# Kernel tuning notes

Measured on AMD Instinct MI355X. Metric: run time of the kernel, lower is better.

## Reference

```python
import jax, jax.numpy as jnp
import numpy as np

N0, N1, N2 = 512, 2048, 8192   # targets, hop1, hop2 node counts
K = 33                          # nneighbor + self loop
IN, HID, OUT, NH = 256, 128, 128, 8
NEG = -9.0e15
ALPHA = 0.2                     # LeakyReLU negative slope


def setup_inputs() -> dict:
    key = jax.random.key(0)
    ks = jax.random.split(key, 8)
    feats = jax.random.normal(ks[0], (N2, IN), jnp.float32)
    # xavier-ish scaled params (gain 1.414)
    W1 = jax.random.normal(ks[1], (NH, IN, HID), jnp.float32) * 0.072
    a1 = jax.random.normal(ks[2], (NH, 2 * HID), jnp.float32) * 0.105
    W2 = jax.random.normal(ks[3], (HID * NH, OUT), jnp.float32) * 0.042
    a2 = jax.random.normal(ks[4], (2 * OUT,), jnp.float32) * 0.105
    # layer1 edges: each of N1 targets gets K distinct neighbors in [0, N2)
    tgt1 = jnp.repeat(jnp.arange(N1, dtype=jnp.int32), K)
    dst1 = ((jnp.arange(N1)[:, None] * 97 + jnp.arange(K)[None, :] * 131) % N2).astype(jnp.int32).reshape(-1)
    src1 = jax.random.randint(ks[5], (N1 * K,), 0, N2, jnp.int32)
    # layer2 edges: each of N0 targets gets K distinct neighbors in [0, N1)
    tgt2 = jnp.repeat(jnp.arange(N0, dtype=jnp.int32), K)
    dst2 = ((jnp.arange(N0)[:, None] * 53 + jnp.arange(K)[None, :] * 61) % N1).astype(jnp.int32).reshape(-1)
    src2 = jax.random.randint(ks[6], (N0 * K,), 0, N1, jnp.int32)
    return dict(feats=feats, W1=W1, a1=a1, W2=W2, a2=a2,
                src1=src1, dst1=dst1, tgt1=tgt1, src2=src2, dst2=dst2, tgt2=tgt2)


def gat_layer(x, W, a, src, dst, tgt, t_len):
    # x: [n, in], W: [in, d], a: [2d]
    h = x @ W                                   # [n, d]
    d = h.shape[1]
    # concat([h[src], h[dst]]) @ a  ==  h[src]@a[:d] + h[dst]@a[d:]
    e = h[src] @ a[:d] + h[dst] @ a[d:]         # [E]
    e = jnp.where(e > 0, e, ALPHA * e)          # LeakyReLU
    att = jnp.full((t_len, h.shape[0]), NEG, h.dtype).at[tgt, dst].set(e)
    att = jax.nn.softmax(att, axis=1)           # dense row softmax (masked entries ~0)
    return jax.nn.elu(att @ h)                  # [t_len, d]


def reference(feats, W1, a1, W2, a2, src1, dst1, tgt1, src2, dst2, tgt2):
    # layer 1: nhead independent GAT heads over hop2 features
    heads = jax.vmap(lambda W, a: gat_layer(feats, W, a, src1, dst1, tgt1, N1))(W1, a1)  # [NH, N1, HID]
    x = jnp.transpose(heads, (1, 0, 2)).reshape(N1, NH * HID)  # torch.cat(dim=1)
    # layer 2: single GAT layer producing [N0, OUT]
    return gat_layer(x, W2, a2, src2, dst2, tgt2, N0)
```

## Files before the change

### kernel.cpp

```cpp
#include <hip/hip_runtime.h>
#include <math.h>

#define ALPHA 0.2f

constexpr int CN0 = 512, CN1 = 2048, CN2 = 8192, CK = 33;
constexpr int CIN = 256, CHID = 128, CNH = 8;

using u16    = unsigned short;
using f32x4  = __attribute__((ext_vector_type(4))) float;
using bf16x8 = __attribute__((ext_vector_type(8))) short;
using short8 = __attribute__((ext_vector_type(8))) short;

__device__ __forceinline__ u16 f2bf(float f) {
    unsigned u = __float_as_uint(f);
    u += 0x7fff + ((u >> 16) & 1);
    return (u16)(u >> 16);
}
__device__ __forceinline__ float bf2f(u16 h) {
    return __uint_as_float(((unsigned)h) << 16);
}

#define GLD16(g, l)                                                        \
    __builtin_amdgcn_global_load_lds(                                      \
        (const __attribute__((address_space(1))) void*)(g),                \
        (__attribute__((address_space(3))) void*)(l), 16, 0, 0)

__global__ __launch_bounds__(256) void prep_k(const float* __restrict__ feats,
                                              u16* __restrict__ fb,
                                              const float* __restrict__ W1,
                                              u16* __restrict__ w1t,
                                              const float* __restrict__ W2,
                                              u16* __restrict__ w2t) {
    __shared__ float t[32][33];
    int b = blockIdx.x;
    if (b < 2048) {
        const int i = (b * 256 + threadIdx.x) * 4;
        const float4 v = *reinterpret_cast<const float4*>(feats + i);
        *reinterpret_cast<ushort4*>(fb + i) =
            make_ushort4(f2bf(v.x), f2bf(v.y), f2bf(v.z), f2bf(v.w));
        return;
    }
    b -= 2048;
    const float* ip;
    u16* op;
    int R, C, r0, c0;
    if (b < 256) {
        const int h = b >> 5, w = b & 31;
        ip = W1 + (size_t)h * CIN * CHID;
        op = w1t + (size_t)h * CIN * CHID;
        R = CIN; C = CHID; r0 = (w >> 2) * 32; c0 = (w & 3) * 32;
    } else {
        b -= 256;
        ip = W2; op = w2t;
        R = CNH * CHID; C = CHID; r0 = (b >> 2) * 32; c0 = (b & 3) * 32;
    }
    const int tx = threadIdx.x & 31, ty = threadIdx.x >> 5;
#pragma unroll
    for (int i = 0; i < 4; ++i)
        t[ty + 8 * i][tx] = ip[(size_t)(r0 + ty + 8 * i) * C + c0 + tx];
    __syncthreads();
#pragma unroll
    for (int i = 0; i < 4; ++i)
        op[(size_t)(c0 + ty + 8 * i) * R + r0 + tx] = f2bf(t[tx][ty + 8 * i]);
}

template <int KSTEPS, bool BF16OUT, bool SCORES>
__global__ __launch_bounds__(256) void gemm_mfma(const u16* __restrict__ A, int lda,
                                                 const u16* __restrict__ Bt, int ldb,
                                                 u16* __restrict__ Cb,
                                                 float* __restrict__ Cf, int ldc,
                                                 long csplit,
                                                 const float* __restrict__ av,
                                                 float* __restrict__ s1o,
                                                 float* __restrict__ s2o,
                                                 int snodes) {
    __shared__ __attribute__((aligned(16))) char smem[24576];

    const int tid  = threadIdx.x;
    const int lane = tid & 63;
    const int wave = tid >> 6;
    const int row0 = blockIdx.x * 64;
    const int col0 = blockIdx.y * 128;
    const int kbase = blockIdx.z * (KSTEPS * 32);
    const int wr = (wave >> 1) * 32;
    const int wc = (wave & 1) * 64;

    f32x4 acc[2][4];
#pragma unroll
    for (int m = 0; m < 2; ++m)
#pragma unroll
        for (int n = 0; n < 4; ++n) acc[m][n] = (f32x4){0.f, 0.f, 0.f, 0.f};

    const int r0c = tid >> 2;
    const int cs0 = tid & 3;
    const int c0  = (cs0 - (r0c >> 1)) & 3;
    const int r1c = r0c + 64;

    const u16* ga0 = A + (size_t)(row0 + r0c) * lda + kbase + c0 * 8;
    const u16* gb0 = Bt + (size_t)(col0 + r0c) * ldb + kbase + c0 * 8;
    const u16* gb1 = Bt + (size_t)(col0 + r1c) * ldb + kbase + c0 * 8;

    auto STAGE = [&](int s) {
        const int k0 = s * 32;
        char* base = smem + (s & 1) * 12288;
        u16* as = (u16*)base + wave * 512;
        u16* bs = (u16*)(base + 4096) + wave * 512;
        GLD16(ga0 + k0, as);
        GLD16(gb0 + k0, bs);
        GLD16(gb1 + k0, bs + 2048);
    };

    STAGE(0);
    __syncthreads();

    for (int s = 0; s < KSTEPS; ++s) {
        if (s + 1 < KSTEPS) STAGE(s + 1);

        const u16* Acur = (const u16*)(smem + (s & 1) * 12288);
        const u16* Bcur = Acur + 2048;

        bf16x8 af[2], bfr[4];
#pragma unroll
        for (int m = 0; m < 2; ++m) {
            const int rt = wr + m * 16 + (lane & 15);
            const int cs = ((lane >> 4) + (rt >> 1)) & 3;
            af[m] = *reinterpret_cast<const bf16x8*>(Acur + rt * 32 + cs * 8);
        }
#pragma unroll
        for (int n = 0; n < 4; ++n) {
            const int rt2 = wc + n * 16 + (lane & 15);
            const int cs2 = ((lane >> 4) + (rt2 >> 1)) & 3;
            bfr[n] = *reinterpret_cast<const bf16x8*>(Bcur + rt2 * 32 + cs2 * 8);
        }
#pragma unroll
        for (int m = 0; m < 2; ++m)
#pragma unroll
            for (int n = 0; n < 4; ++n)
                acc[m][n] = __builtin_amdgcn_mfma_f32_16x16x32_bf16(
                    af[m], bfr[n], acc[m][n], 0, 0, 0);

        __syncthreads();
    }

    if constexpr (BF16OUT) {
        u16* Cs = (u16*)smem;
#pragma unroll
        for (int m = 0; m < 2; ++m) {
            const int rr = wr + m * 16 + (lane >> 4) * 4;
#pragma unroll
            for (int n = 0; n < 4; ++n) {
                const int cc = wc + n * 16 + (lane & 15);
#pragma unroll
                for (int q = 0; q < 4; ++q)
                    Cs[(rr + q) * 136 + cc] = f2bf(acc[m][n][q]);
            }
        }
        __syncthreads();
#pragma unroll
        for (int i = 0; i < 4; ++i) {
            const int cid = i * 256 + tid;
            const int r  = cid >> 4;
            const int kc = cid & 15;
            const int4 v = *reinterpret_cast<const int4*>(&Cs[r * 136 + kc * 8]);
            *reinterpret_cast<int4*>(&Cb[(long)(row0 + r) * ldc + col0 + kc * 8]) = v;
        }
    } else {
        const long cbase = (long)blockIdx.z * csplit;
#pragma unroll
        for (int m = 0; m < 2; ++m) {
            const int rr = row0 + wr + m * 16 + (lane >> 4) * 4;
#pragma unroll
            for (int n = 0; n < 4; ++n) {
                const int cc = col0 + wc + n * 16 + (lane & 15);
#pragma unroll
                for (int q = 0; q < 4; ++q)
                    Cf[cbase + (long)(rr + q) * ldc + cc] = acc[m][n][q];
            }
        }
    }

    if constexpr (SCORES) {
        __shared__ float sred1[2][64];
        __shared__ float sred2[2][64];
        const int head = blockIdx.y;
        float av1[4], av2[4];
#pragma unroll
        for (int n = 0; n < 4; ++n) {
            const int c = wc + n * 16 + (lane & 15);
            av1[n] = av[head * 2 * CHID + c];
            av2[n] = av[head * 2 * CHID + CHID + c];
        }
        float p1[2][4], p2[2][4];
#pragma unroll
        for (int m = 0; m < 2; ++m)
#pragma unroll
            for (int q = 0; q < 4; ++q) {
                float t1 = 0.f, t2 = 0.f;
#pragma unroll
                for (int n = 0; n < 4; ++n) {
                    t1 = fmaf(acc[m][n][q], av1[n], t1);
                    t2 = fmaf(acc[m][n][q], av2[n], t2);
                }
#pragma unroll
                for (int mk = 1; mk < 16; mk <<= 1) {
                    t1 += __shfl_xor(t1, mk);
                    t2 += __shfl_xor(t2, mk);
                }
                p1[m][q] = t1;
                p2[m][q] = t2;
            }
        if ((lane & 15) == 0) {
            const int g = lane >> 4;
#pragma unroll
            for (int m = 0; m < 2; ++m)
#pragma unroll
                for (int q = 0; q < 4; ++q) {
                    sred1[wave & 1][wr + m * 16 + g * 4 + q] = p1[m][q];
                    sred2[wave & 1][wr + m * 16 + g * 4 + q] = p2[m][q];
                }
        }
        __syncthreads();
        if (tid < 64) {
            s1o[head * snodes + row0 + tid] = sred1[0][tid] + sred1[1][tid];
            s2o[head * snodes + row0 + tid] = sred2[0][tid] + sred2[1][tid];
        }
    }
}

__global__ __launch_bounds__(128) void agg1_k(const float* __restrict__ s1,
                                              const float* __restrict__ s2,
                                              const int* __restrict__ src,
                                              const int* __restrict__ dst,
                                              const u16* __restrict__ hm,
                                              u16* __restrict__ xout) {
    __shared__ float wgt[CNH][CK];
    __shared__ int dsts[CK];

    const int t    = blockIdx.x;
    const int tid  = threadIdx.x;
    const int wv   = tid >> 6;
    const int lane = tid & 63;

    int sv = 0, dv = 0;
    if (lane < CK) {
        sv = src[t * CK + lane];
        dv = dst[t * CK + lane];
        if (tid < CK) dsts[tid] = dv;
    }
#pragma unroll
    for (int hh = 0; hh < 4; ++hh) {
        const int head = wv * 4 + hh;
        float e = -3.0e38f;
        if (lane < CK) {
            const float ee = s1[head * CN2 + sv] + s2[head * CN2 + dv];
            e = (ee > 0.f) ? ee : ALPHA * ee;
        }
        float m = e;
#pragma unroll
        for (int mm = 1; mm < 64; mm <<= 1) m = fmaxf(m, __shfl_xor(m, mm));
        const float p = (lane < CK) ? __expf(e - m) : 0.f;
        float s = p;
#pragma unroll
        for (int mm = 1; mm < 64; mm <<= 1) s += __shfl_xor(s, mm);
        if (lane < CK) wgt[head][lane] = p / s;
    }
    __syncthreads();

    const int c0   = tid * 8;
    const int head = tid >> 4;
    float acc[8] = {0.f, 0.f, 0.f, 0.f, 0.f, 0.f, 0.f, 0.f};
#pragma unroll
    for (int k = 0; k < CK; ++k) {
        const short8 hv = *reinterpret_cast<const short8*>(
            hm + (size_t)dsts[k] * (CNH * CHID) + c0);
        const float w = wgt[head][k];
#pragma unroll
        for (int j = 0; j < 8; ++j) acc[j] = fmaf(w, bf2f((u16)hv[j]), acc[j]);
    }
    short8 o;
#pragma unroll
    for (int j = 0; j < 8; ++j) {
        const float v = (acc[j] > 0.f) ? acc[j] : __expf(acc[j]) - 1.f;
        o[j] = (short)f2bf(v);
    }
    *reinterpret_cast<short8*>(xout + (size_t)t * (CNH * CHID) + c0) = o;
}

__global__ __launch_bounds__(256) void scores2_k(const float* __restrict__ part,
                                                 const float* __restrict__ a,
                                                 float* __restrict__ h2,
                                                 float* __restrict__ s1,
                                                 float* __restrict__ s2) {
    const int wid  = (blockIdx.x * 256 + threadIdx.x) >> 6;
    const int lane = threadIdx.x & 63;
    const int j = lane * 2;
    float x0 = 0.f, x1 = 0.f;
#pragma unroll
    for (int sp = 0; sp < 8; ++sp) {
        const float2 v = *reinterpret_cast<const float2*>(
            part + (size_t)sp * CN1 * CHID + (size_t)wid * CHID + j);
        x0 += v.x; x1 += v.y;
    }
    *reinterpret_cast<float2*>(h2 + (size_t)wid * CHID + j) = make_float2(x0, x1);
    float d1 = x0 * a[j] + x1 * a[j + 1];
    float d2 = x0 * a[CHID + j] + x1 * a[CHID + j + 1];
#pragma unroll
    for (int m = 1; m < 64; m <<= 1) {
        d1 += __shfl_xor(d1, m);
        d2 += __shfl_xor(d2, m);
    }
    if (lane == 0) { s1[wid] = d1; s2[wid] = d2; }
}

__global__ __launch_bounds__(256) void agg2_k(const float* __restrict__ s1,
                                              const float* __restrict__ s2,
                                              const int* __restrict__ src,
                                              const int* __restrict__ dst,
                                              const float* __restrict__ h2,
                                              float* __restrict__ out) {
    const int t    = (blockIdx.x * 256 + threadIdx.x) >> 6;
    const int lane = threadIdx.x & 63;

    float e = -3.0e38f;
    int dv = 0;
    if (lane < CK) {
        const int sv = src[t * CK + lane];
        dv = dst[t * CK + lane];
        const float ee = s1[sv] + s2[dv];
        e = (ee > 0.f) ? ee : ALPHA * ee;
    }
    float m = e;
#pragma unroll
    for (int mm = 1; mm < 64; mm <<= 1) m = fmaxf(m, __shfl_xor(m, mm));
    float p = (lane < CK) ? __expf(e - m) : 0.f;
    float ssum = p;
#pragma unroll
    for (int mm = 1; mm < 64; mm <<= 1) ssum += __shfl_xor(ssum, mm);
    const float invs = 1.f / ssum;

    float a0 = 0.f, a1 = 0.f;
#pragma unroll
    for (int k = 0; k < CK; ++k) {
        const float w = __shfl(p, k) * invs;
        const int d = __shfl(dv, k);
        const float2 hv = *reinterpret_cast<const float2*>(h2 + (size_t)d * CHID + lane * 2);
        a0 = fmaf(w, hv.x, a0);
        a1 = fmaf(w, hv.y, a1);
    }
    a0 = (a0 > 0.f) ? a0 : __expf(a0) - 1.f;
    a1 = (a1 > 0.f) ? a1 : __expf(a1) - 1.f;
    *reinterpret_cast<float2*>(out + (size_t)t * CHID + lane * 2) = make_float2(a0, a1);
}

extern "C" void kernel_launch(void* const* d_in, const int* in_sizes, int n_in,
                              void* d_out, int out_size, void* d_ws, size_t ws_size,
                              hipStream_t stream) {
    const float* feats = (const float*)d_in[0];
    const float* W1    = (const float*)d_in[1];
    const float* a1    = (const float*)d_in[2];
    const float* W2    = (const float*)d_in[3];
    const float* a2    = (const float*)d_in[4];
    const int*   src1  = (const int*)d_in[5];
    const int*   dst1  = (const int*)d_in[6];
    const int*   src2  = (const int*)d_in[8];
    const int*   dst2  = (const int*)d_in[9];
    float* out = (float*)d_out;

    char* w = (char*)d_ws;
    u16*   fb   = (u16*)w;                 w += (size_t)CN2 * CIN * 2;
    u16*   w1t  = (u16*)w;                 w += (size_t)CNH * CIN * CHID * 2;
    u16*   w2t  = (u16*)w;                 w += (size_t)CNH * CHID * CHID * 2;
    u16*   h1b  = (u16*)w;                 w += (size_t)CN2 * CNH * CHID * 2;
    float* s1   = (float*)w;               w += (size_t)CNH * CN2 * 4;
    float* s2   = (float*)w;               w += (size_t)CNH * CN2 * 4;
    u16*   xb   = (u16*)w;                 w += (size_t)CN1 * CNH * CHID * 2;
    float* part = (float*)w;               w += (size_t)8 * CN1 * CHID * 4;
    float* h2   = (float*)w;               w += (size_t)CN1 * CHID * 4;
    float* s21  = (float*)w;               w += (size_t)CN1 * 4;
    float* s22  = (float*)w;               w += (size_t)CN1 * 4;

    prep_k<<<dim3(2048 + 256 + 128), 256, 0, stream>>>(feats, fb, W1, w1t, W2, w2t);

    gemm_mfma<8, true, true><<<dim3(CN2 / 64, (CNH * CHID) / 128), 256, 0, stream>>>(
        fb, CIN, w1t, CIN, h1b, nullptr, CNH * CHID, 0, a1, s1, s2, CN2);

    agg1_k<<<dim3(CN1), 128, 0, stream>>>(s1, s2, src1, dst1, h1b, xb);

    gemm_mfma<4, false, false><<<dim3(CN1 / 64, 1, 8), 256, 0, stream>>>(
        xb, CNH * CHID, w2t, CNH * CHID, nullptr, part, CHID, (long)CN1 * CHID,
        nullptr, nullptr, nullptr, 0);

    scores2_k<<<dim3(CN1 / 4), 256, 0, stream>>>(part, a2, h2, s21, s22);

    agg2_k<<<dim3(CN0 / 4), 256, 0, stream>>>(s21, s22, src2, dst2, h2, out);
}
```

Baseline: 60.51 us.

## Replace split-K partial buffer with atomics and fuse layer-2 scores into aggregation

Result: slower. 80.94 us (+33.8%).

```diff
diff --git a/kernel.cpp b/kernel.cpp
--- a/kernel.cpp
+++ b/kernel.cpp
@@ -30,7 +30,8 @@
                                               const float* __restrict__ W1,
                                               u16* __restrict__ w1t,
                                               const float* __restrict__ W2,
-                                              u16* __restrict__ w2t) {
+                                              u16* __restrict__ w2t,
+                                              float* __restrict__ h2) {
     __shared__ float t[32][33];
     int b = blockIdx.x;
     if (b < 2048) {
@@ -38,6 +39,13 @@
         const float4 v = *reinterpret_cast<const float4*>(feats + i);
         *reinterpret_cast<ushort4*>(fb + i) =
             make_ushort4(f2bf(v.x), f2bf(v.y), f2bf(v.z), f2bf(v.w));
+        return;
+    }
+    if (b >= 2432) {
+        const int i = ((b - 2432) * 256 + threadIdx.x) * 8;
+        const float4 z = make_float4(0.f, 0.f, 0.f, 0.f);
+        *reinterpret_cast<float4*>(h2 + i)     = z;
+        *reinterpret_cast<float4*>(h2 + i + 4) = z;
         return;
     }
     b -= 2048;
@@ -69,7 +77,6 @@
                                                  const u16* __restrict__ Bt, int ldb,
                                                  u16* __restrict__ Cb,
                                                  float* __restrict__ Cf, int ldc,
-                                                 long csplit,
                                                  const float* __restrict__ av,
                                                  float* __restrict__ s1o,
                                                  float* __restrict__ s2o,
@@ -79,8 +86,8 @@
     const int tid  = threadIdx.x;
     const int lane = tid & 63;
     const int wave = tid >> 6;
-    const int row0 = blockIdx.x * 64;
-    const int col0 = blockIdx.y * 128;
+    const int row0 = blockIdx.y * 64;
+    const int col0 = blockIdx.x * 128;
     const int kbase = blockIdx.z * (KSTEPS * 32);
     const int wr = (wave >> 1) * 32;
     const int wc = (wave & 1) * 64;
@@ -165,7 +172,6 @@
             *reinterpret_cast<int4*>(&Cb[(long)(row0 + r) * ldc + col0 + kc * 8]) = v;
         }
     } else {
-        const long cbase = (long)blockIdx.z * csplit;
 #pragma unroll
         for (int m = 0; m < 2; ++m) {
             const int rr = row0 + wr + m * 16 + (lane >> 4) * 4;
@@ -174,7 +180,7 @@
                 const int cc = col0 + wc + n * 16 + (lane & 15);
 #pragma unroll
                 for (int q = 0; q < 4; ++q)
-                    Cf[cbase + (long)(rr + q) * ldc + cc] = acc[m][n][q];
+                    atomicAdd(&Cf[(long)(rr + q) * ldc + cc], acc[m][n][q]);
             }
         }
     }
@@ -182,7 +188,7 @@
     if constexpr (SCORES) {
         __shared__ float sred1[2][64];
         __shared__ float sred2[2][64];
-        const int head = blockIdx.y;
+        const int head = blockIdx.x;
         float av1[4], av2[4];
 #pragma unroll
         for (int n = 0; n < 4; ++n) {
@@ -286,70 +292,57 @@
     *reinterpret_cast<short8*>(xout + (size_t)t * (CNH * CHID) + c0) = o;
 }
 
-__global__ __launch_bounds__(256) void scores2_k(const float* __restrict__ part,
-                                                 const float* __restrict__ a,
-                                                 float* __restrict__ h2,
-                                                 float* __restrict__ s1,
-                                                 float* __restrict__ s2) {
-    const int wid  = (blockIdx.x * 256 + threadIdx.x) >> 6;
-    const int lane = threadIdx.x & 63;
-    const int j = lane * 2;
-    float x0 = 0.f, x1 = 0.f;
-#pragma unroll
-    for (int sp = 0; sp < 8; ++sp) {
-        const float2 v = *reinterpret_cast<const float2*>(
-            part + (size_t)sp * CN1 * CHID + (size_t)wid * CHID + j);
-        x0 += v.x; x1 += v.y;
-    }
-    *reinterpret_cast<float2*>(h2 + (size_t)wid * CHID + j) = make_float2(x0, x1);
-    float d1 = x0 * a[j] + x1 * a[j + 1];
-    float d2 = x0 * a[CHID + j] + x1 * a[CHID + j + 1];
-#pragma unroll
-    for (int m = 1; m < 64; m <<= 1) {
-        d1 += __shfl_xor(d1, m);
-        d2 += __shfl_xor(d2, m);
-    }
-    if (lane == 0) { s1[wid] = d1; s2[wid] = d2; }
-}
-
-__global__ __launch_bounds__(256) void agg2_k(const float* __restrict__ s1,
-                                              const float* __restrict__ s2,
-                                              const int* __restrict__ src,
-                                              const int* __restrict__ dst,
-                                              const float* __restrict__ h2,
-                                              float* __restrict__ out) {
-    const int t    = (blockIdx.x * 256 + threadIdx.x) >> 6;
-    const int lane = threadIdx.x & 63;
-
-    float e = -3.0e38f;
-    int dv = 0;
-    if (lane < CK) {
-        const int sv = src[t * CK + lane];
-        dv = dst[t * CK + lane];
-        const float ee = s1[sv] + s2[dv];
-        e = (ee > 0.f) ? ee : ALPHA * ee;
-    }
-    float m = e;
-#pragma unroll
-    for (int mm = 1; mm < 64; mm <<= 1) m = fmaxf(m, __shfl_xor(m, mm));
-    float p = (lane < CK) ? __expf(e - m) : 0.f;
-    float ssum = p;
-#pragma unroll
-    for (int mm = 1; mm < 64; mm <<= 1) ssum += __shfl_xor(ssum, mm);
-    const float invs = 1.f / ssum;
-
-    float a0 = 0.f, a1 = 0.f;
-#pragma unroll
+__global__ __launch_bounds__(128) void final_k(const float* __restrict__ h2,
+                                               const float* __restrict__ a2,
+                                               const int* __restrict__ src,
+                                               const int* __restrict__ dst,
+                                               float* __restrict__ out) {
+    __shared__ float e1[CK], e2[CK], wgt[CK];
+    __shared__ int dsts[CK];
+
+    const int t    = blockIdx.x;
+    const int tid  = threadIdx.x;
+    const int wv   = tid >> 6;
+    const int lane = tid & 63;
+
+    const float* ap = a2 + wv * CHID + lane * 2;
+    const float a0 = ap[0], a1v = ap[1];
     for (int k = 0; k < CK; ++k) {
-        const float w = __shfl(p, k) * invs;
-        const int d = __shfl(dv, k);
-        const float2 hv = *reinterpret_cast<const float2*>(h2 + (size_t)d * CHID + lane * 2);
-        a0 = fmaf(w, hv.x, a0);
-        a1 = fmaf(w, hv.y, a1);
-    }
-    a0 = (a0 > 0.f) ? a0 : __expf(a0) - 1.f;
-    a1 = (a1 > 0.f) ? a1 : __expf(a1) - 1.f;
-    *reinterpret_cast<float2*>(out + (size_t)t * CHID + lane * 2) = make_float2(a0, a1);
+        const int node = (wv == 0) ? src[t * CK + k] : dst[t * CK + k];
+        const float2 hv = *reinterpret_cast<const float2*>(
+            h2 + (size_t)node * CHID + lane * 2);
+        float d = hv.x * a0 + hv.y * a1v;
+#pragma unroll
+        for (int m = 1; m < 64; m <<= 1) d += __shfl_xor(d, m);
+        if (lane == 0) {
+            if (wv == 0) e1[k] = d;
+            else { e2[k] = d; dsts[k] = node; }
+        }
+    }
+    __syncthreads();
+
+    if (tid < 64) {
+        float e = -3.0e38f;
+        if (tid < CK) {
+            const float ee = e1[tid] + e2[tid];
+            e = (ee > 0.f) ? ee : ALPHA * ee;
+        }
+        float m = e;
+#pragma unroll
+        for (int mm = 1; mm < 64; mm <<= 1) m = fmaxf(m, __shfl_xor(m, mm));
+        const float p = (tid < CK) ? __expf(e - m) : 0.f;
+        float s = p;
+#pragma unroll
+        for (int mm = 1; mm < 64; mm <<= 1) s += __shfl_xor(s, mm);
+        if (tid < CK) wgt[tid] = p / s;
+    }
+    __syncthreads();
+
+    float acc = 0.f;
+#pragma unroll
+    for (int k = 0; k < CK; ++k)
+        acc = fmaf(wgt[k], h2[(size_t)dsts[k] * CHID + tid], acc);
+    out[(size_t)t * CHID + tid] = (acc > 0.f) ? acc : __expf(acc) - 1.f;
 }
 
 extern "C" void kernel_launch(void* const* d_in, const int* in_sizes, int n_in,
@@ -374,23 +367,19 @@
     float* s1   = (float*)w;               w += (size_t)CNH * CN2 * 4;
     float* s2   = (float*)w;               w += (size_t)CNH * CN2 * 4;
     u16*   xb   = (u16*)w;                 w += (size_t)CN1 * CNH * CHID * 2;
-    float* part = (float*)w;               w += (size_t)8 * CN1 * CHID * 4;
     float* h2   = (float*)w;               w += (size_t)CN1 * CHID * 4;
-    float* s21  = (float*)w;               w += (size_t)CN1 * 4;
-    float* s22  = (float*)w;               w += (size_t)CN1 * 4;
-
-    prep_k<<<dim3(2048 + 256 + 128), 256, 0, stream>>>(feats, fb, W1, w1t, W2, w2t);
-
-    gemm_mfma<8, true, true><<<dim3(CN2 / 64, (CNH * CHID) / 128), 256, 0, stream>>>(
-        fb, CIN, w1t, CIN, h1b, nullptr, CNH * CHID, 0, a1, s1, s2, CN2);
+
+    prep_k<<<dim3(2048 + 256 + 128 + 128), 256, 0, stream>>>(
+        feats, fb, W1, w1t, W2, w2t, h2);
+
+    gemm_mfma<8, true, true><<<dim3((CNH * CHID) / 128, CN2 / 64), 256, 0, stream>>>(
+        fb, CIN, w1t, CIN, h1b, nullptr, CNH * CHID, a1, s1, s2, CN2);
 
     agg1_k<<<dim3(CN1), 128, 0, stream>>>(s1, s2, src1, dst1, h1b, xb);
 
-    gemm_mfma<4, false, false><<<dim3(CN1 / 64, 1, 8), 256, 0, stream>>>(
-        xb, CNH * CHID, w2t, CNH * CHID, nullptr, part, CHID, (long)CN1 * CHID,
+    gemm_mfma<4, false, false><<<dim3(1, CN1 / 64, 8), 256, 0, stream>>>(
+        xb, CNH * CHID, w2t, CNH * CHID, nullptr, h2, CHID,
         nullptr, nullptr, nullptr, 0);
 
-    scores2_k<<<dim3(CN1 / 4), 256, 0, stream>>>(part, a2, h2, s21, s22);
-
-    agg2_k<<<dim3(CN0 / 4), 256, 0, stream>>>(s21, s22, src2, dst2, h2, out);
-}
+    final_k<<<dim3(CN0), 128, 0, stream>>>(h2, a2, src2, dst2, out);
+}
```
